# Kernel optimization log

Hardware: AMD Instinct MI355X
Metric: run time of the kernel (lower is better)

## Reference

```python
import jax, jax.numpy as jnp
import numpy as np

N_HEADS = 32
N_KV_HEADS = 8
HEAD_DIM = 64


def _apply_rope(x, cos, sin):
    # x: [b, s, h, d]; cos/sin: [s, d//2]; interleaved real/imag pairs
    xr = x[..., 0::2]
    xi = x[..., 1::2]
    c = cos[None, :, None, :]
    s = sin[None, :, None, :]
    out_r = xr * c - xi * s
    out_i = xr * s + xi * c
    return jnp.stack([out_r, out_i], axis=-1).reshape(x.shape)


def setup_inputs() -> dict:
    key = jax.random.key(0)
    ks = jax.random.split(key, 10)
    b, s, dim = 2, 512, 2048
    cache_len = 1536
    half = HEAD_DIM // 2
    pos = jnp.arange(cache_len, cache_len + s, dtype=jnp.float32)
    inv_freq = 1.0 / (10000.0 ** (jnp.arange(0, half, dtype=jnp.float32) / half))
    ang = pos[:, None] * inv_freq[None, :]
    scale = 0.02
    return {
        "x": jax.random.normal(ks[0], (b, s, dim), jnp.float32),
        "freqs_cos": jnp.cos(ang),
        "freqs_sin": jnp.sin(ang),
        "k_cache": jax.random.normal(ks[1], (b, N_KV_HEADS, cache_len, HEAD_DIM), jnp.float32),
        "v_cache": jax.random.normal(ks[2], (b, N_KV_HEADS, cache_len, HEAD_DIM), jnp.float32),
        "attn_mask": jnp.zeros((s, cache_len + s), jnp.float32),
        "wq": jax.random.normal(ks[3], (N_HEADS * HEAD_DIM, dim), jnp.float32) * scale,
        "wk": jax.random.normal(ks[4], (N_KV_HEADS * HEAD_DIM, dim), jnp.float32) * scale,
        "wv": jax.random.normal(ks[5], (N_KV_HEADS * HEAD_DIM, dim), jnp.float32) * scale,
        "wo": jax.random.normal(ks[6], (dim, N_HEADS * HEAD_DIM), jnp.float32) * scale,
    }


def reference(x, freqs_cos, freqs_sin, k_cache, v_cache, attn_mask, wq, wk, wv, wo):
    b, s, dim = x.shape
    n_rep = N_HEADS // N_KV_HEADS
    # QKV projections (nn.Linear: y = x @ W.T)
    q = (x @ wq.T).reshape(b, s, N_HEADS, HEAD_DIM)
    k = (x @ wk.T).reshape(b, s, N_KV_HEADS, HEAD_DIM)
    v = (x @ wv.T).reshape(b, s, N_KV_HEADS, HEAD_DIM)
    # RoPE on q, k
    q = _apply_rope(q, freqs_cos, freqs_sin)
    k = _apply_rope(k, freqs_cos, freqs_sin)
    # [b, h, s, d]
    q = q.transpose(0, 2, 1, 3)
    k = k.transpose(0, 2, 1, 3)
    v = v.transpose(0, 2, 1, 3)
    new_k, new_v = k, v
    # KV-cache concat along sequence dim
    k_full = jnp.concatenate([k_cache, k], axis=2)
    v_full = jnp.concatenate([v_cache, v], axis=2)
    # GQA: repeat_interleave kv heads
    if n_rep > 1:
        k_full = jnp.repeat(k_full, n_rep, axis=1)
        v_full = jnp.repeat(v_full, n_rep, axis=1)
    # SDPA
    scale = 1.0 / jnp.sqrt(jnp.asarray(HEAD_DIM, x.dtype))
    scores = jnp.einsum("bhqd,bhkd->bhqk", q, k_full) * scale + attn_mask
    probs = jax.nn.softmax(scores, axis=-1)
    out = jnp.einsum("bhqk,bhkd->bhqd", probs, v_full)
    out = out.transpose(0, 2, 1, 3).reshape(b, s, N_HEADS * HEAD_DIM)
    out = out @ wo.T
    return (out, new_k, new_v)
```

## Files before the change

kernel.cpp:

```cpp
#include <hip/hip_runtime.h>
#include <hip/hip_bf16.h>

typedef __attribute__((ext_vector_type(8))) short bf16x8;
typedef __attribute__((ext_vector_type(4))) float f32x4;
typedef unsigned short u16;

#define MFMA16(a, b, c) __builtin_amdgcn_mfma_f32_16x16x32_bf16(a, b, c, 0, 0, 0)
#define GLL(srcp, dstp) __builtin_amdgcn_global_load_lds(                      \
    (const __attribute__((address_space(1))) void*)(srcp),                     \
    (__attribute__((address_space(3))) void*)(dstp), 16, 0, 0)

__device__ __forceinline__ u16 f2b(float f) {
  union { float f; unsigned u; } a; a.f = f;
  return (u16)((a.u + 0x7FFFu + ((a.u >> 16) & 1u)) >> 16);
}
__device__ __forceinline__ unsigned pk2(float lo, float hi) {
  __hip_bfloat162 h = __float22bfloat162_rn(make_float2(lo, hi));
  return *reinterpret_cast<unsigned*>(&h);
}

__global__ __launch_bounds__(256) void prep(const float* __restrict__ x,
                                            const float* __restrict__ kc,
                                            u16* __restrict__ xb,
                                            u16* __restrict__ kfull) {
  const int c = blockIdx.x * 256 + threadIdx.x;
  const float* src;
  u16* dst;
  if (c < 524288) {
    src = x + (size_t)c * 4; dst = xb + (size_t)c * 4;
  } else {
    int l = c - 524288;
    int bh = l / 24576, r = l - bh * 24576;
    src = kc + (size_t)bh * 98304 + (size_t)r * 4;
    dst = kfull + (size_t)bh * 131072 + (size_t)r * 4;
  }
  const float4 v = *(const float4*)src;
  ushort4 o;
  o.x = f2b(v.x); o.y = f2b(v.y); o.z = f2b(v.z); o.w = f2b(v.w);
  *(ushort4*)dst = o;
}

__global__ __launch_bounds__(256) void vtr(const float* __restrict__ vc,
                                           const float* __restrict__ newv,
                                           u16* __restrict__ vT) {
  __shared__ float tile[64][65];
  const int kt = blockIdx.x, bh = blockIdx.y;
  const float* src;
  int colbase;
  if (kt < 24) {
    src = vc + ((size_t)bh * 1536 + (size_t)kt * 64) * 64;
    colbase = kt * 64;
  } else {
    src = newv + ((size_t)bh * 512 + (size_t)(kt - 24) * 64) * 64;
    colbase = 1536 + (kt - 24) * 64;
  }
  const int t = threadIdx.x;
#pragma unroll
  for (int j = 0; j < 4; j++) {
    int e = t + j * 256;
    int r = e >> 4, c = (e & 15) * 4;
    float4 v = *(const float4*)(src + (size_t)r * 64 + c);
    tile[r][c] = v.x; tile[r][c + 1] = v.y; tile[r][c + 2] = v.z; tile[r][c + 3] = v.w;
  }
  __syncthreads();
  int d = t >> 2, kv0 = (t & 3) * 16;
  u16* dst = vT + ((size_t)bh * 64 + d) * 2048 + colbase + kv0;
#pragma unroll
  for (int i = 0; i < 16; i++) dst[i] = f2b(tile[kv0 + i][d]);
}

__global__ __launch_bounds__(256, 3) void gemm_bt(const u16* __restrict__ A,
                                                  const float* __restrict__ B0,
                                                  const float* __restrict__ B1,
                                                  const float* __restrict__ B2,
                                                  float* __restrict__ Cp,
                                                  int M, int N, int K, int nb1, int nb2) {
  __shared__ __attribute__((aligned(16))) u16 As[2][4096];
  __shared__ __attribute__((aligned(16))) u16 Bs[2][8192];
  const int t = threadIdx.x;
  const int lane = t & 63, w = t >> 6;
  const int wr = (w >> 1) * 32, wc = (w & 1) * 64;
  const int g = lane >> 4, cc = lane & 15;
  const int nby = N >> 7, cpx = nby >> 3, nrt = M >> 6;
  const int j = blockIdx.x & 7, q = blockIdx.x >> 3;
  const int ct = j * cpx + (q % cpx);
  const int rest = q / cpx;
  const int rt = rest % nrt, ks = rest / nrt;
  const size_t row0 = (size_t)rt * 64;
  const int col0 = ct * 128;
  const int k0base = ks * (K >> 1);

  const int lr = lane >> 3, lc = lane & 7;
  const int swz = lc ^ lr;
  const u16* aS = A + (row0 + w * 16 + lr) * (size_t)K + swz * 8 + k0base;
  const float* Bb;
  int brow;
  if (col0 < nb1) { Bb = B0; brow = col0; }
  else if (col0 < nb2) { Bb = B1; brow = col0 - nb1; }
  else { Bb = B2; brow = col0 - nb2; }
  const float* bS = Bb + (brow + w * 32 + lr) * (size_t)K + swz * 8 + k0base;

  f32x4 acc[2][4] = {};
  f32x4 blA[4][2], blB[4][2];

#define ALOAD(bufi, kk0)                                                       \
  {                                                                            \
    _Pragma("unroll") for (int i = 0; i < 2; i++)                              \
        GLL(aS + (size_t)(i * 8) * K + (kk0), &As[bufi][(w * 16 + i * 8) * 64]); \
  }
#define BLOAD(blv, kk0)                                                        \
  {                                                                            \
    _Pragma("unroll") for (int i = 0; i < 4; i++) {                            \
      blv[i][0] = *(const f32x4*)(bS + (size_t)(i * 8) * K + (kk0));           \
      blv[i][1] = *(const f32x4*)(bS + (size_t)(i * 8) * K + (kk0) + 4);       \
    }                                                                          \
  }
#define BWRITE(blv, bufi)                                                      \
  {                                                                            \
    _Pragma("unroll") for (int i = 0; i < 4; i++) {                            \
      uint4 pw;                                                                \
      pw.x = pk2(blv[i][0][0], blv[i][0][1]);                                  \
      pw.y = pk2(blv[i][0][2], blv[i][0][3]);                                  \
      pw.z = pk2(blv[i][1][0], blv[i][1][1]);                                  \
      pw.w = pk2(blv[i][1][2], blv[i][1][3]);                                  \
      *(uint4*)&Bs[bufi][(w * 32 + i * 8 + lr) * 64 + lc * 8] = pw;            \
    }                                                                          \
  }

  const int niter = (K >> 1) >> 6;

  ALOAD(0, 0);
  BLOAD(blA, 0);
  BWRITE(blA, 0);
  BLOAD(blB, 64);
  asm volatile("s_waitcnt lgkmcnt(0)" ::: "memory");
  __builtin_amdgcn_s_barrier();

#define GBODY(it_, blPrev, blCur)                                              \
  {                                                                            \
    const int buf = (it_) & 1;                                                 \
    if ((it_) > 0) {                                                           \
      if ((it_) + 1 < niter) {                                                 \
        asm volatile("s_waitcnt vmcnt(8)" ::: "memory");                       \
      } else {                                                                 \
        asm volatile("s_waitcnt vmcnt(0)" ::: "memory");                       \
      }                                                                        \
      asm volatile("s_waitcnt lgkmcnt(0)" ::: "memory");                       \
      __builtin_amdgcn_s_barrier();                                            \
    }                                                                          \
    if ((it_) + 1 < niter) ALOAD(buf ^ 1, ((it_) + 1) * 64);                   \
    if ((it_) + 2 < niter) BLOAD(blCur, ((it_) + 2) * 64);                     \
    bf16x8 av[2][2], bv[4][2];                                                 \
    _Pragma("unroll") for (int m = 0; m < 2; m++) {                            \
      const int row = wr + m * 16 + cc;                                        \
      _Pragma("unroll") for (int kk = 0; kk < 2; kk++)                         \
          av[m][kk] =                                                          \
              *(const bf16x8*)(&As[buf][row * 64 + (((kk * 4 + g) ^ (cc & 7)) * 8)]); \
    }                                                                          \
    _Pragma("unroll") for (int n = 0; n < 4; n++) {                            \
      const int row = wc + n * 16 + cc;                                        \
      _Pragma("unroll") for (int kk = 0; kk < 2; kk++)                         \
          bv[n][kk] =                                                          \
              *(const bf16x8*)(&Bs[buf][row * 64 + (((kk * 4 + g) ^ (cc & 7)) * 8)]); \
    }                                                                          \
    _Pragma("unroll") for (int kk = 0; kk < 2; kk++)                           \
        _Pragma("unroll") for (int m = 0; m < 2; m++)                          \
        _Pragma("unroll") for (int n = 0; n < 4; n++)                          \
            acc[m][n] = MFMA16(av[m][kk], bv[n][kk], acc[m][n]);               \
    if ((it_) + 1 < niter) BWRITE(blPrev, buf ^ 1);                            \
  }

  for (int it = 0; it < niter; it += 2) {
    GBODY(it, blB, blA);
    GBODY(it + 1, blA, blB);
  }
#undef GBODY
#undef ALOAD
#undef BLOAD
#undef BWRITE

  float* Cw = Cp + (size_t)ks * M * N;
#pragma unroll
  for (int m = 0; m < 2; m++)
#pragma unroll
    for (int n = 0; n < 4; n++)
#pragma unroll
      for (int r = 0; r < 4; r++)
        Cw[(row0 + wr + m * 16 + g * 4 + r) * N + (col0 + wc + n * 16 + cc)] = acc[m][n][r];
}

__global__ __launch_bounds__(256) void postproc(const float* __restrict__ Cp0,
                                                const float* __restrict__ Cp1,
                                                const float* __restrict__ fcos,
                                                const float* __restrict__ fsin,
                                                u16* __restrict__ qrope,
                                                u16* __restrict__ kfull,
                                                float* __restrict__ newk,
                                                float* __restrict__ newv) {
  int idx = blockIdx.x * 256 + threadIdx.x;
  if (idx >= 1024 * 1536) return;
  int m = idx / 1536, p = idx - m * 1536;
  int b = m >> 9, s = m & 511;
  const float* r0 = Cp0 + (size_t)m * 3072;
  const float* r1 = Cp1 + (size_t)m * 3072;
  if (p < 1280) {
    bool isq = p < 1024;
    int pk = isq ? p : p - 1024;
    int h = pk >> 5, i = pk & 31;
    int colbase = (isq ? 0 : 2048) + h * 64 + 2 * i;
    float xr = r0[colbase] + r1[colbase];
    float xi = r0[colbase + 1] + r1[colbase + 1];
    float co = fcos[s * 32 + i], si = fsin[s * 32 + i];
    float orr = xr * co - xi * si;
    float oii = xr * si + xi * co;
    if (isq) {
      u16* dst = qrope + (((size_t)(b * 32 + h) * 512 + s) * 64 + 2 * i);
      dst[0] = f2b(orr); dst[1] = f2b(oii);
    } else {
      size_t o0 = ((size_t)(b * 8 + h) * 512 + s) * 64 + 2 * i;
      newk[o0] = orr; newk[o0 + 1] = oii;
      u16* kf = kfull + (((size_t)(b * 8 + h) * 2048 + 1536 + s) * 64 + 2 * i);
      kf[0] = f2b(orr); kf[1] = f2b(oii);
    }
  } else {
    int pv = p - 1280;
    int h = pv >> 5, i = pv & 31;
    int cb = 2560 + h * 64 + 2 * i;
    float v0 = r0[cb] + r1[cb], v1 = r0[cb + 1] + r1[cb + 1];
    size_t o0 = ((size_t)(b * 8 + h) * 512 + s) * 64 + 2 * i;
    newv[o0] = v0; newv[o0 + 1] = v1;
  }
}

__global__ __launch_bounds__(256) void sumout(const float* __restrict__ a,
                                              const float* __restrict__ b,
                                              float* __restrict__ out) {
  const int i = blockIdx.x * 256 + threadIdx.x;
  const float4 va = *(const float4*)(a + (size_t)i * 4);
  const float4 vb = *(const float4*)(b + (size_t)i * 4);
  float4 o;
  o.x = va.x + vb.x; o.y = va.y + vb.y; o.z = va.z + vb.z; o.w = va.w + vb.w;
  *(float4*)(out + (size_t)i * 4) = o;
}

__global__ __launch_bounds__(512, 4) void attn_split(const u16* __restrict__ qrope,
                                                     const u16* __restrict__ kfull,
                                                     const u16* __restrict__ vT,
                                                     const float* __restrict__ mask,
                                                     float* __restrict__ po,
                                                     float* __restrict__ ml) {
  __shared__ __attribute__((aligned(16))) u16 Ks[4][4096];
  __shared__ __attribute__((aligned(16))) u16 Vs[4][4096];
  __shared__ __attribute__((aligned(16))) u16 P_lds[8192];
  const int t = threadIdx.x, lane = t & 63, w = t >> 6;
  const int g = lane >> 4, cc = lane & 15;
  const int p = blockIdx.x;
  const int v = (p & 7) * 64 + (p >> 3);
  const int bh = v >> 3, qt = (v >> 1) & 3, sp = v & 1;
  const int b = bh >> 5, h = bh & 31;
  const int bhkv = b * 8 + (h >> 2);
  const int s0 = qt * 128 + w * 16;
  const int j0beg = sp * 1024;

  const int lr = lane >> 3, lc = lane & 7;
  const int swzc = lc ^ lr;

  bf16x8 qa0, qa1;
  {
    const u16* qb = qrope + ((size_t)bh * 512 + s0 + cc) * 64 + g * 8;
    qa0 = *(const bf16x8*)qb;
    qa1 = *(const bf16x8*)(qb + 32);
  }
  float mrow[4], lsum[4];
  f32x4 o[4] = {};
#pragma unroll
  for (int r = 0; r < 4; r++) { mrow[r] = -1e30f; lsum[r] = 0.0f; }

  u16* Pw = P_lds + w * 1024;
  const float* mbase = mask + (size_t)(s0 + g * 4) * 2048 + cc;
  const u16* ksrc0 = kfull + (size_t)bhkv * 131072 + (size_t)(w * 8 + lr) * 64 + swzc * 8;
  const u16* vsrc0 = vT + ((size_t)bhkv * 64 + w * 8 + lr) * 2048 + swzc * 8;

#pragma unroll
  for (int pt = 0; pt < 3; ++pt) {
    GLL(ksrc0 + (size_t)(j0beg + pt * 64) * 64, &Ks[pt][w * 512]);
    GLL(vsrc0 + (j0beg + pt * 64), &Vs[pt][w * 512]);
  }

  for (int it = 0; it < 16; ++it) {
    const int buf = it & 3;
    const int j0 = j0beg + it * 64;
    if (it < 14) {
      asm volatile("s_waitcnt vmcnt(4)" ::: "memory");
    } else if (it == 14) {
      asm volatile("s_waitcnt vmcnt(2)" ::: "memory");
    } else {
      asm volatile("s_waitcnt vmcnt(0)" ::: "memory");
    }
    __builtin_amdgcn_s_barrier();

    float mk[4][4];
#pragma unroll
    for (int r = 0; r < 4; r++)
#pragma unroll
      for (int jb = 0; jb < 4; jb++)
        mk[r][jb] = mbase[(size_t)r * 2048 + j0 + jb * 16];
    __builtin_amdgcn_sched_barrier(0);
    if (it < 13) {
      GLL(ksrc0 + (size_t)(j0 + 192) * 64, &Ks[(it + 3) & 3][w * 512]);
      GLL(vsrc0 + (j0 + 192), &Vs[(it + 3) & 3][w * 512]);
    }

    f32x4 sc[4];
    __builtin_amdgcn_s_setprio(1);
#pragma unroll
    for (int jb = 0; jb < 4; jb++) {
      const bf16x8 k0 = *(const bf16x8*)(&Ks[buf][(jb * 16 + cc) * 64 + ((g ^ (cc & 7)) * 8)]);
      const bf16x8 k1 =
          *(const bf16x8*)(&Ks[buf][(jb * 16 + cc) * 64 + (((g + 4) ^ (cc & 7)) * 8)]);
      f32x4 z = {0.f, 0.f, 0.f, 0.f};
      z = MFMA16(qa0, k0, z);
      z = MFMA16(qa1, k1, z);
      sc[jb] = z;
    }
    __builtin_amdgcn_s_setprio(0);
    float pp[4][4];
#pragma unroll
    for (int r = 0; r < 4; r++) {
#pragma unroll
      for (int jb = 0; jb < 4; jb++)
        pp[r][jb] = sc[jb][r] * 0.125f + mk[r][jb];
      const float lm = fmaxf(fmaxf(pp[r][0], pp[r][1]), fmaxf(pp[r][2], pp[r][3]));
      if (__any(lm > mrow[r] + 8.0f)) {
        float tm = lm;
#pragma unroll
        for (int off = 1; off < 16; off <<= 1) tm = fmaxf(tm, __shfl_xor(tm, off, 64));
        const float newm = fmaxf(mrow[r], tm);
        const float corr = __expf(mrow[r] - newm);
        mrow[r] = newm;
        lsum[r] *= corr;
#pragma unroll
        for (int db = 0; db < 4; db++) o[db][r] *= corr;
      }
      float ps = 0.f;
#pragma unroll
      for (int jb = 0; jb < 4; jb++) { pp[r][jb] = __expf(pp[r][jb] - mrow[r]); ps += pp[r][jb]; }
      lsum[r] += ps;
      const int rowb = (g * 4 + r) * 128;
      const int sw = ((g * 4 + r) & 7) << 4;
#pragma unroll
      for (int jb = 0; jb < 4; jb++)
        Pw[((rowb + (jb * 16 + cc) * 2) ^ sw) >> 1] = f2b(pp[r][jb]);
    }
    __builtin_amdgcn_s_setprio(1);
#pragma unroll
    for (int kk = 0; kk < 2; kk++) {
      const bf16x8 pa =
          *(const bf16x8*)(Pw + (((cc * 128 + kk * 64 + g * 16) ^ ((cc & 7) << 4)) >> 1));
#pragma unroll
      for (int db = 0; db < 4; db++) {
        const bf16x8 vf =
            *(const bf16x8*)(&Vs[buf][(db * 16 + cc) * 64 + (((kk * 4 + g) ^ (cc & 7)) * 8)]);
        o[db] = MFMA16(pa, vf, o[db]);
      }
    }
    __builtin_amdgcn_s_setprio(0);
  }
#pragma unroll
  for (int r = 0; r < 4; r++) {
    float ps = lsum[r];
#pragma unroll
    for (int off = 1; off < 16; off <<= 1) ps += __shfl_xor(ps, off, 64);
    const size_t row = (size_t)bh * 512 + s0 + g * 4 + r;
    float* dst = po + (row * 2 + sp) * 64 + cc;
#pragma unroll
    for (int db = 0; db < 4; db++) dst[db * 16] = o[db][r];
    if (cc == 0) {
      float2* mlp = (float2*)ml;
      mlp[row * 2 + sp] = make_float2(mrow[r], ps);
    }
  }
}

__global__ __launch_bounds__(256) void attn_combine(const float* __restrict__ po,
                                                    const float* __restrict__ ml,
                                                    u16* __restrict__ aout) {
  const int t = threadIdx.x;
  const int row = blockIdx.x * 4 + (t >> 6);
  const int d = t & 63;
  const int bh = row >> 9, s = row & 511;
  const int b = bh >> 5, h = bh & 31;
  const float2* mlp = (const float2*)ml;
  const float2 m0 = mlp[row * 2 + 0], m1 = mlp[row * 2 + 1];
  const float M = fmaxf(m0.x, m1.x);
  const float w0 = __expf(m0.x - M), w1 = __expf(m1.x - M);
  const float L = m0.y * w0 + m1.y * w1;
  const float o = po[(size_t)(row * 2 + 0) * 64 + d] * w0 +
                  po[(size_t)(row * 2 + 1) * 64 + d] * w1;
  aout[((size_t)(b * 512 + s)) * 2048 + h * 64 + d] = f2b(o / L);
}

extern "C" void kernel_launch(void* const* d_in, const int* in_sizes, int n_in,
                              void* d_out, int out_size, void* d_ws, size_t ws_size,
                              hipStream_t stream) {
  (void)in_sizes; (void)n_in; (void)out_size; (void)ws_size;
  const float* x    = (const float*)d_in[0];
  const float* fcos = (const float*)d_in[1];
  const float* fsin = (const float*)d_in[2];
  const float* kc   = (const float*)d_in[3];
  const float* vc   = (const float*)d_in[4];
  const float* mask = (const float*)d_in[5];
  const float* wq   = (const float*)d_in[6];
  const float* wk   = (const float*)d_in[7];
  const float* wv   = (const float*)d_in[8];
  const float* wo   = (const float*)d_in[9];

  float* out_f = (float*)d_out;
  float* newk  = out_f + 2097152;
  float* newv  = out_f + 2621440;

  u16*   xb    = (u16*)d_ws;
  float* Cp    = (float*)(xb + 2097152);
  float* Cp1   = Cp + 3145728;
  u16*   qrope = (u16*)(Cp + 6291456);
  u16*   kfull = qrope + 2097152;
  u16*   vTf   = kfull + 2097152;
  u16*   aout  = vTf + 2097152;
  float* ml    = (float*)(aout + 2097152);
  float* po    = (float*)d_ws;
  float* Co    = (float*)d_ws;
  float* Co1   = Co + 2097152;

  prep<<<3584, 256, 0, stream>>>(x, kc, xb, kfull);

  gemm_bt<<<768, 256, 0, stream>>>(xb, wq, wk, wv, Cp,
                                   1024, 3072, 2048, 2048, 2560);
  postproc<<<6144, 256, 0, stream>>>(Cp, Cp1, fcos, fsin, qrope, kfull, newk, newv);
  vtr<<<dim3(32, 16), 256, 0, stream>>>(vc, newv, vTf);
  attn_split<<<512, 512, 0, stream>>>(qrope, kfull, vTf, mask, po, ml);
  attn_combine<<<8192, 256, 0, stream>>>(po, ml, aout);
  gemm_bt<<<512, 256, 0, stream>>>(aout, wo, wo, wo, Co,
                                   1024, 2048, 2048, 4096, 8192);
  sumout<<<2048, 256, 0, stream>>>(Co, Co1, out_f);
}
```

Measured before the change: 124.2 us.

## Split attention KV range four ways with double-buffered tiles and packed P stores

The attention kernel becomes templated on the number of KV splits. When the workspace is large enough it runs four splits, doubling the block count, and the combine kernel merges any number of partials. K/V staging drops from a 4-deep to a 2-deep LDS ring so more blocks fit per CU, at the cost of less prefetch depth and a full vmcnt(0) wait each iteration. The P tile is now written as packed 8-byte stores, and the V transpose kernel writes columns in a matching permuted key order so the P·V product stays correct.

Measured after the change: 242.7 us. 1.95x slower.

```diff
diff --git a/kernel.cpp b/kernel.cpp
--- a/kernel.cpp
+++ b/kernel.cpp
@@ -64,9 +64,9 @@
   }
   __syncthreads();
   int d = t >> 2, kv0 = (t & 3) * 16;
-  u16* dst = vT + ((size_t)bh * 64 + d) * 2048 + colbase + kv0;
-#pragma unroll
-  for (int i = 0; i < 16; i++) dst[i] = f2b(tile[kv0 + i][d]);
+  u16* dst = vT + ((size_t)bh * 64 + d) * 2048 + colbase + (kv0 >> 4);
+#pragma unroll
+  for (int i = 0; i < 16; i++) dst[i * 4] = f2b(tile[kv0 + i][d]);
 }
 
 __global__ __launch_bounds__(256, 3) void gemm_bt(const u16* __restrict__ A,
@@ -243,24 +243,28 @@
   *(float4*)(out + (size_t)i * 4) = o;
 }
 
-__global__ __launch_bounds__(512, 4) void attn_split(const u16* __restrict__ qrope,
+template <int NSP>
+__global__ __launch_bounds__(512, 6) void attn_split(const u16* __restrict__ qrope,
                                                      const u16* __restrict__ kfull,
                                                      const u16* __restrict__ vT,
                                                      const float* __restrict__ mask,
                                                      float* __restrict__ po,
                                                      float* __restrict__ ml) {
-  __shared__ __attribute__((aligned(16))) u16 Ks[4][4096];
-  __shared__ __attribute__((aligned(16))) u16 Vs[4][4096];
+  __shared__ __attribute__((aligned(16))) u16 Ks[2][4096];
+  __shared__ __attribute__((aligned(16))) u16 Vs[2][4096];
   __shared__ __attribute__((aligned(16))) u16 P_lds[8192];
   const int t = threadIdx.x, lane = t & 63, w = t >> 6;
   const int g = lane >> 4, cc = lane & 15;
   const int p = blockIdx.x;
-  const int v = (p & 7) * 64 + (p >> 3);
-  const int bh = v >> 3, qt = (v >> 1) & 3, sp = v & 1;
+  const int v = (p & 7) * (32 * NSP) + (p >> 3);
+  const int bh = v / (4 * NSP);
+  const int rem = v & (4 * NSP - 1);
+  const int qt = rem / NSP, sp = rem & (NSP - 1);
   const int b = bh >> 5, h = bh & 31;
   const int bhkv = b * 8 + (h >> 2);
   const int s0 = qt * 128 + w * 16;
-  const int j0beg = sp * 1024;
+  constexpr int NIT = 32 / NSP;
+  const int j0beg = sp * (NIT * 64);
 
   const int lr = lane >> 3, lc = lane & 7;
   const int swzc = lc ^ lr;
@@ -281,22 +285,13 @@
   const u16* ksrc0 = kfull + (size_t)bhkv * 131072 + (size_t)(w * 8 + lr) * 64 + swzc * 8;
   const u16* vsrc0 = vT + ((size_t)bhkv * 64 + w * 8 + lr) * 2048 + swzc * 8;
 
-#pragma unroll
-  for (int pt = 0; pt < 3; ++pt) {
-    GLL(ksrc0 + (size_t)(j0beg + pt * 64) * 64, &Ks[pt][w * 512]);
-    GLL(vsrc0 + (j0beg + pt * 64), &Vs[pt][w * 512]);
-  }
-
-  for (int it = 0; it < 16; ++it) {
-    const int buf = it & 3;
+  GLL(ksrc0 + (size_t)j0beg * 64, &Ks[0][w * 512]);
+  GLL(vsrc0 + j0beg, &Vs[0][w * 512]);
+
+  for (int it = 0; it < NIT; ++it) {
+    const int buf = it & 1;
     const int j0 = j0beg + it * 64;
-    if (it < 14) {
-      asm volatile("s_waitcnt vmcnt(4)" ::: "memory");
-    } else if (it == 14) {
-      asm volatile("s_waitcnt vmcnt(2)" ::: "memory");
-    } else {
-      asm volatile("s_waitcnt vmcnt(0)" ::: "memory");
-    }
+    asm volatile("s_waitcnt vmcnt(0)" ::: "memory");
     __builtin_amdgcn_s_barrier();
 
     float mk[4][4];
@@ -306,9 +301,9 @@
       for (int jb = 0; jb < 4; jb++)
         mk[r][jb] = mbase[(size_t)r * 2048 + j0 + jb * 16];
     __builtin_amdgcn_sched_barrier(0);
-    if (it < 13) {
-      GLL(ksrc0 + (size_t)(j0 + 192) * 64, &Ks[(it + 3) & 3][w * 512]);
-      GLL(vsrc0 + (j0 + 192), &Vs[(it + 3) & 3][w * 512]);
+    if (it + 1 < NIT) {
+      GLL(ksrc0 + (size_t)(j0 + 64) * 64, &Ks[buf ^ 1][w * 512]);
+      GLL(vsrc0 + (j0 + 64), &Vs[buf ^ 1][w * 512]);
     }
 
     f32x4 sc[4];
@@ -348,9 +343,10 @@
       lsum[r] += ps;
       const int rowb = (g * 4 + r) * 128;
       const int sw = ((g * 4 + r) & 7) << 4;
-#pragma unroll
-      for (int jb = 0; jb < 4; jb++)
-        Pw[((rowb + (jb * 16 + cc) * 2) ^ sw) >> 1] = f2b(pp[r][jb]);
+      uint2 pw;
+      pw.x = pk2(pp[r][0], pp[r][1]);
+      pw.y = pk2(pp[r][2], pp[r][3]);
+      *(uint2*)((char*)Pw + ((rowb + cc * 8) ^ sw)) = pw;
     }
     __builtin_amdgcn_s_setprio(1);
 #pragma unroll
@@ -372,16 +368,17 @@
 #pragma unroll
     for (int off = 1; off < 16; off <<= 1) ps += __shfl_xor(ps, off, 64);
     const size_t row = (size_t)bh * 512 + s0 + g * 4 + r;
-    float* dst = po + (row * 2 + sp) * 64 + cc;
+    float* dst = po + (row * NSP + sp) * 64 + cc;
 #pragma unroll
     for (int db = 0; db < 4; db++) dst[db * 16] = o[db][r];
     if (cc == 0) {
       float2* mlp = (float2*)ml;
-      mlp[row * 2 + sp] = make_float2(mrow[r], ps);
-    }
-  }
-}
-
+      mlp[row * NSP + sp] = make_float2(mrow[r], ps);
+    }
+  }
+}
+
+template <int NSP>
 __global__ __launch_bounds__(256) void attn_combine(const float* __restrict__ po,
                                                     const float* __restrict__ ml,
                                                     u16* __restrict__ aout) {
@@ -391,19 +388,24 @@
   const int bh = row >> 9, s = row & 511;
   const int b = bh >> 5, h = bh & 31;
   const float2* mlp = (const float2*)ml;
-  const float2 m0 = mlp[row * 2 + 0], m1 = mlp[row * 2 + 1];
-  const float M = fmaxf(m0.x, m1.x);
-  const float w0 = __expf(m0.x - M), w1 = __expf(m1.x - M);
-  const float L = m0.y * w0 + m1.y * w1;
-  const float o = po[(size_t)(row * 2 + 0) * 64 + d] * w0 +
-                  po[(size_t)(row * 2 + 1) * 64 + d] * w1;
+  float2 mv[NSP];
+  float M = -1e30f;
+#pragma unroll
+  for (int i = 0; i < NSP; i++) { mv[i] = mlp[row * NSP + i]; M = fmaxf(M, mv[i].x); }
+  float L = 0.f, o = 0.f;
+#pragma unroll
+  for (int i = 0; i < NSP; i++) {
+    const float wgt = __expf(mv[i].x - M);
+    L += mv[i].y * wgt;
+    o += po[(size_t)(row * NSP + i) * 64 + d] * wgt;
+  }
   aout[((size_t)(b * 512 + s)) * 2048 + h * 64 + d] = f2b(o / L);
 }
 
 extern "C" void kernel_launch(void* const* d_in, const int* in_sizes, int n_in,
                               void* d_out, int out_size, void* d_ws, size_t ws_size,
                               hipStream_t stream) {
-  (void)in_sizes; (void)n_in; (void)out_size; (void)ws_size;
+  (void)in_sizes; (void)n_in; (void)out_size;
   const float* x    = (const float*)d_in[0];
   const float* fcos = (const float*)d_in[1];
   const float* fsin = (const float*)d_in[2];
@@ -419,10 +421,13 @@
   float* newk  = out_f + 2097152;
   float* newv  = out_f + 2621440;
 
-  u16*   xb    = (u16*)d_ws;
-  float* Cp    = (float*)(xb + 2097152);
-  float* Cp1   = Cp + 3145728;
-  u16*   qrope = (u16*)(Cp + 6291456);
+  const bool big = ws_size >= (size_t)50 * 1024 * 1024;
+
+  u16*   xb  = (u16*)d_ws;
+  float* Cp  = (float*)(xb + 2097152);
+  float* Cp1 = Cp + 3145728;
+  u16*   qrope = big ? (u16*)((char*)d_ws + (size_t)32 * 1048576)
+                     : (u16*)(Cp + 6291456);
   u16*   kfull = qrope + 2097152;
   u16*   vTf   = kfull + 2097152;
   u16*   aout  = vTf + 2097152;
@@ -437,8 +442,13 @@
                                    1024, 3072, 2048, 2048, 2560);
   postproc<<<6144, 256, 0, stream>>>(Cp, Cp1, fcos, fsin, qrope, kfull, newk, newv);
   vtr<<<dim3(32, 16), 256, 0, stream>>>(vc, newv, vTf);
-  attn_split<<<512, 512, 0, stream>>>(qrope, kfull, vTf, mask, po, ml);
-  attn_combine<<<8192, 256, 0, stream>>>(po, ml, aout);
+  if (big) {
+    attn_split<4><<<1024, 512, 0, stream>>>(qrope, kfull, vTf, mask, po, ml);
+    attn_combine<4><<<8192, 256, 0, stream>>>(po, ml, aout);
+  } else {
+    attn_split<2><<<512, 512, 0, stream>>>(qrope, kfull, vTf, mask, po, ml);
+    attn_combine<2><<<8192, 256, 0, stream>>>(po, ml, aout);
+  }
   gemm_bt<<<512, 256, 0, stream>>>(aout, wo, wo, wo, Co,
                                    1024, 2048, 2048, 4096, 8192);
   sumout<<<2048, 256, 0, stream>>>(Co, Co1, out_f);
```
